# Optimization experiments

Hardware: AMD Instinct MI355X
Metric: run time of the kernel (lower is better)

The kernel has to match this reference:

```python
import jax, jax.numpy as jnp
import numpy as np

B, L, DIM = 16, 4096, 512
N_FFT, HOP, WIN = 1024, 256, 1024
PAD = (WIN - HOP) // 2  # 'same' padding trim
OUT_DIM = N_FFT + 2


def hann_window(win):
    n = jnp.arange(win, dtype=jnp.float32)
    return 0.5 - 0.5 * jnp.cos(2.0 * jnp.pi * n / win)


def setup_inputs() -> dict:
    key = jax.random.key(0)
    k1, k2 = jax.random.split(key)
    x = jax.random.normal(k1, (B, L, DIM), dtype=jnp.float32)
    W = jax.random.normal(k2, (OUT_DIM, DIM), dtype=jnp.float32) * 0.02
    b = jnp.zeros((OUT_DIM,), dtype=jnp.float32)
    return {"x": x, "W": W, "b": b}


def _istft(S):
    # S: (B, N_FFT//2+1, T) complex rfft spectrum
    T = S.shape[-1]
    frames = jnp.fft.irfft(S, n=N_FFT, axis=1)
    window = hann_window(WIN)
    frames = frames * window[None, :, None]
    out_len = (T - 1) * HOP + WIN
    idx = jnp.arange(T)[:, None] * HOP + jnp.arange(WIN)[None, :]
    fr = frames.transpose(0, 2, 1)
    y = jnp.zeros((fr.shape[0], out_len), fr.dtype).at[:, idx].add(fr)
    env = jnp.zeros((out_len,), fr.dtype).at[idx].add(
        jnp.broadcast_to(window * window, idx.shape))
    y = y[:, PAD:out_len - PAD]
    env = env[PAD:out_len - PAD]
    return y / env


def reference(x, W, b):
    # Linear projection: (B, L, DIM) -> (B, L, N_FFT+2)
    h = jnp.einsum('bld,od->blo', x, W) + b
    h = h.transpose(0, 2, 1)                              # (B, N_FFT+2, L)
    mag, p = jnp.split(h, 2, axis=1)                      # each (B, N_FFT//2+1, L)
    mag = jnp.minimum(jnp.exp(mag), 100.0)                # exp + clip(max=100)
    S = mag * jax.lax.complex(jnp.cos(p), jnp.sin(p))
    return _istft(S)                                      # (B, L*HOP)
```

## Files before the change

### kernel.cpp

```cpp
#include <hip/hip_runtime.h>
#include <hip/hip_bf16.h>
#include <math.h>

#define BATCH   16
#define TFRM    4096
#define DIM     512
#define NFFT    1024
#define HOP     256
#define PADC    384
#define MROWS   (BATCH*TFRM)
#define OUTLEN  1048576
#define TWO_PI_OVER_N 0.006135923151542565f
#define INV_TWO_PI    0.15915494309189535f

typedef __bf16 bf16x8 __attribute__((ext_vector_type(8)));
typedef float  f32x4  __attribute__((ext_vector_type(4)));

__device__ __forceinline__ ushort f2bf(float f) {
  union { float f; unsigned u; } v; v.f = f;
  unsigned u = v.u;
  unsigned r = (u + 0x7FFFu + ((u >> 16) & 1u)) >> 16;
  return (ushort)r;
}
__device__ __forceinline__ float bf2f(ushort h) {
  union { unsigned u; float f; } v; v.u = ((unsigned)h) << 16;
  return v.f;
}
__device__ __forceinline__ float fast_sin(float x) { return __builtin_amdgcn_sinf(x * INV_TWO_PI); }
__device__ __forceinline__ float fast_cos(float x) { return __builtin_amdgcn_cosf(x * INV_TWO_PI); }
__device__ __forceinline__ float fast_exp(float x) { return __builtin_amdgcn_exp2f(x * 1.4426950408889634f); }
__device__ __forceinline__ float dpp_xor1(float v) {
  return __int_as_float(__builtin_amdgcn_update_dpp(
      __float_as_int(v), __float_as_int(v), 0xB1, 0xF, 0xF, false));
}

__global__ void k_prep_x(const float* __restrict__ x, const float* __restrict__ W,
                         const float* __restrict__ bias,
                         ushort* __restrict__ xbf, float* __restrict__ s512) {
  const int row  = blockIdx.x * 4 + (threadIdx.x >> 6);
  const int lane = threadIdx.x & 63;
  const float* xr = x + (size_t)row * DIM + lane * 8;
  float4 v0 = *(const float4*)xr;
  float4 v1 = *(const float4*)(xr + 4);
  ushort4 u0, u1;
  u0.x = f2bf(v0.x); u0.y = f2bf(v0.y); u0.z = f2bf(v0.z); u0.w = f2bf(v0.w);
  u1.x = f2bf(v1.x); u1.y = f2bf(v1.y); u1.z = f2bf(v1.z); u1.w = f2bf(v1.w);
  ushort* xo = xbf + (size_t)row * DIM + lane * 8;
  *(ushort4*)xo = u0;
  *(ushort4*)(xo + 4) = u1;
  const float* w0 = W + 512 * DIM + lane * 8;
  const float* w1 = W + 1025 * DIM + lane * 8;
  float4 a0 = *(const float4*)w0, a1 = *(const float4*)(w0 + 4);
  float4 b0 = *(const float4*)w1, b1 = *(const float4*)(w1 + 4);
  float sm = v0.x*a0.x + v0.y*a0.y + v0.z*a0.z + v0.w*a0.w
           + v1.x*a1.x + v1.y*a1.y + v1.z*a1.z + v1.w*a1.w;
  float sp = v0.x*b0.x + v0.y*b0.y + v0.z*b0.z + v0.w*b0.w
           + v1.x*b1.x + v1.y*b1.y + v1.z*b1.z + v1.w*b1.w;
#pragma unroll
  for (int off = 32; off; off >>= 1) {
    sm += __shfl_down(sm, off);
    sp += __shfl_down(sp, off);
  }
  if (lane == 0) {
    float mag = fminf(fast_exp(sm + bias[512]), 100.0f);
    s512[row] = mag * fast_cos(sp + bias[1025]) * (1.0f / 1024.0f);
  }
}

__global__ void k_prep_w(const float* __restrict__ W, ushort* __restrict__ o) {
  int i = blockIdx.x * 256 + threadIdx.x;
  int r = i >> 9;
  int c = i & 511;
  int orig = (r >> 1) + (r & 1) * 513;
  o[i] = f2bf(W[orig * DIM + c]);
}

__global__ void k_basis(ushort* __restrict__ basE, ushort* __restrict__ basO) {
  int r = blockIdx.x;
  int n = r + 1;
  for (int k = threadIdx.x; k < 512; k += 256) {
    float e, o;
    if (k == 0) { e = 1.0f / 1024.0f; o = 0.0f; }
    else {
      int ph = (k * n) & 1023;
      float ang = (float)ph * TWO_PI_OVER_N;
      e = 2.0f * cosf(ang) * (1.0f / 1024.0f);
      o = 2.0f * sinf(ang) * (1.0f / 1024.0f);
    }
    basE[r * 512 + k] = f2bf(e);
    basO[r * 512 + k] = f2bf(o);
  }
}

template<int EPI>
__global__ __launch_bounds__(256) void k_gemm(const ushort* A, const ushort* A2, int lda,
                                              const ushort* Bt, const ushort* Bt2, int ldb,
                                              ushort* C, ushort* C2, int ldc,
                                              int nbn, int NK, int nsplit,
                                              const float* __restrict__ bias,
                                              const float* __restrict__ s512) {
  __shared__ __align__(16) ushort lds[3][2][128 * 32];
  const int tid  = threadIdx.x;
  const int cpx  = gridDim.x >> 3;
  int bid  = (blockIdx.x & 7) * cpx + (blockIdx.x >> 3);
  bool second = false;
  if (nsplit > 0 && bid >= nsplit) { second = true; A = A2; Bt = Bt2; C = C2; bid -= nsplit; }
  const int bm   = bid / nbn;
  const int bn   = bid - bm * nbn;
  const int lane = tid & 63;
  const int wv   = tid >> 6;
  const int wr   = (wv >> 1) * 64;
  const int wc   = (wv & 1) * 64;
  const int lr   = lane & 15;
  const int gx   = ((lane >> 4) ^ ((lane >> 1) & 3)) << 3;

  f32x4 acc[4][4] = {};

  const int swz = ((tid & 3) ^ ((tid >> 3) & 3)) << 3;
  auto stage = [&](const ushort* __restrict__ g, int ld, int row0, int k0, ushort* l) {
#pragma unroll
    for (int p = 0; p < 2; ++p) {
      int i = tid + p * 256;
      const ushort* gp = g + (size_t)(row0 + (i >> 2)) * ld + k0 + swz;
      ushort* lp = l + ((i >> 6) << 9);
      __builtin_amdgcn_global_load_lds(
          (const __attribute__((address_space(1))) void*)gp,
          (__attribute__((address_space(3))) void*)lp, 16, 0, 0);
    }
  };

  stage(A,  lda, bm * 128, 0,  &lds[0][0][0]);
  stage(Bt, ldb, bn * 128, 0,  &lds[0][1][0]);
  stage(A,  lda, bm * 128, 32, &lds[1][0][0]);
  stage(Bt, ldb, bn * 128, 32, &lds[1][1][0]);
  asm volatile("s_waitcnt vmcnt(4)" ::: "memory");
  __syncthreads();

  int sl = 0;
  for (int t = 0; t < NK; ++t) {
    if (t + 2 < NK) {
      const int psl = (sl >= 1) ? sl - 1 : 2;
      stage(A,  lda, bm * 128, (t + 2) << 5, &lds[psl][0][0]);
      stage(Bt, ldb, bn * 128, (t + 2) << 5, &lds[psl][1][0]);
    }
    const ushort* lA = &lds[sl][0][0];
    const ushort* lB = &lds[sl][1][0];
    bf16x8 aF[4], bF[4];
#pragma unroll
    for (int m = 0; m < 4; ++m)
      aF[m] = *(const bf16x8*)(lA + (wr + m * 16 + lr) * 32 + gx);
#pragma unroll
    for (int n = 0; n < 4; ++n)
      bF[n] = *(const bf16x8*)(lB + (wc + n * 16 + lr) * 32 + gx);
#pragma unroll
    for (int m = 0; m < 4; ++m)
#pragma unroll
      for (int n = 0; n < 4; ++n)
        acc[m][n] = __builtin_amdgcn_mfma_f32_16x16x32_bf16(aF[m], bF[n], acc[m][n], 0, 0, 0);
    if (t + 2 < NK)      asm volatile("s_waitcnt vmcnt(4)" ::: "memory");
    else if (t + 2 == NK) asm volatile("s_waitcnt vmcnt(0)" ::: "memory");
    if (t + 1 < NK) __syncthreads();
    sl = (sl >= 2) ? 0 : sl + 1;
  }

  const int rl = wr + ((lane >> 4) << 2);
  const int r0 = bm * 128 + rl;
  ushort* epi = &lds[0][0][0];
  __syncthreads();

  if constexpr (EPI == 0) {
#pragma unroll
    for (int m = 0; m < 4; ++m) {
      float4 sv4 = {0.f, 0.f, 0.f, 0.f};
      if (!second) sv4 = *(const float4*)(s512 + r0 + m * 16);
#pragma unroll
      for (int j = 0; j < 4; ++j) {
        float sv = ((const float*)&sv4)[j];
        int row = rl + m * 16 + j;
#pragma unroll
        for (int n = 0; n < 4; ++n) {
          int c = wc + n * 16 + lr;
          float par = second ? 0.0f : ((c & 1) ? sv : -sv);
          epi[row * 144 + c] = f2bf(acc[m][n][j] + par);
        }
      }
    }
    __syncthreads();
#pragma unroll
    for (int i = 0; i < 8; ++i) {
      int row = (tid >> 4) + i * 16;
      int co  = (tid & 15) << 3;
      bf16x8 v = *(const bf16x8*)(epi + row * 144 + co);
      *(bf16x8*)(C + (size_t)(bm * 128 + row) * ldc + bn * 128 + co) = v;
    }
  } else {
    ushort* tA = epi;
    ushort* tB = epi + 128 * 80;
#pragma unroll
    for (int m = 0; m < 4; ++m) {
#pragma unroll
      for (int n = 0; n < 4; ++n) {
        const int cl  = wc + n * 16 + lr;
        const int kk  = (bn * 128 + cl) >> 1;
        const bool isPhase = (cl & 1);
        const float bs = bias[isPhase ? 513 + kk : kk];
        ushort* dst = (isPhase ? tB : tA);
        const int kkl = cl >> 1;
#pragma unroll
        for (int j = 0; j < 4; ++j) {
          float v = acc[m][n][j] + bs;
          float pv = dpp_xor1(v);
          float hm = isPhase ? pv : v;
          float hp = isPhase ? v : pv;
          float mag = fminf(fast_exp(hm), 100.0f);
          float outv = isPhase ? mag * fast_sin(hp) : mag * fast_cos(hp);
          dst[(rl + m * 16 + j) * 80 + kkl] = f2bf(outv);
        }
      }
    }
    __syncthreads();
#pragma unroll
    for (int i = 0; i < 4; ++i) {
      int row = (tid >> 3) + i * 32;
      int co  = (tid & 7) << 3;
      size_t go = (size_t)(bm * 128 + row) * ldc + bn * 64 + co;
      bf16x8 va = *(const bf16x8*)(tA + row * 80 + co);
      *(bf16x8*)(C + go) = va;
      bf16x8 vb = *(const bf16x8*)(tB + row * 80 + co);
      *(bf16x8*)(C2 + go) = vb;
    }
  }
}

__global__ void k_oa(const ushort* __restrict__ E, const ushort* __restrict__ O,
                     float* __restrict__ out) {
  int u = blockIdx.x * 256 + threadIdx.x;
  int b  = u >> 18;
  int g  = u & 262143;
  int s  = (g << 2) + PADC;
  int t0 = s >> 8;
  int nb = s & 255;
  float acc[4] = {0.f, 0.f, 0.f, 0.f};
  bool interior = (t0 >= 3) && (t0 < TFRM);
  float env[4];
#pragma unroll
  for (int j = 0; j < 4; ++j) env[j] = interior ? 1.5f : 0.0f;
#pragma unroll
  for (int q = 0; q < 4; ++q) {
    int t = t0 - q;
    if (t < 0 || t >= TFRM) continue;
    int n = nb + (q << 8);
    size_t base = ((size_t)(b << 12) + t) << 9;
    float w[4];
#pragma unroll
    for (int j = 0; j < 4; ++j) {
      w[j] = 0.5f - 0.5f * __builtin_amdgcn_cosf((float)(n + j) * (1.0f / 1024.0f));
      if (!interior) env[j] += w[j] * w[j];
    }
    float d[4];
    if (n <= 508) {
      ushort4 e1 = *(const ushort4*)(E + base + n);
      ushort4 o1 = *(const ushort4*)(O + base + n);
      if (n >= 4) {
        ushort4 e0 = *(const ushort4*)(E + base + n - 4);
        ushort4 o0 = *(const ushort4*)(O + base + n - 4);
        d[0] = bf2f(e0.w) - bf2f(o0.w);
      } else d[0] = 0.0f;
      d[1] = bf2f(e1.x) - bf2f(o1.x);
      d[2] = bf2f(e1.y) - bf2f(o1.y);
      d[3] = bf2f(e1.z) - bf2f(o1.z);
    } else if (n == 512) {
      ushort4 e = *(const ushort4*)(E + base + 508);
      ushort4 o = *(const ushort4*)(O + base + 508);
      d[0] = bf2f(e.w) - bf2f(o.w);
      d[1] = bf2f(e.z) + bf2f(o.z);
      d[2] = bf2f(e.y) + bf2f(o.y);
      d[3] = bf2f(e.x) + bf2f(o.x);
    } else {
      ushort4 e = *(const ushort4*)(E + base + 1020 - n);
      ushort4 o = *(const ushort4*)(O + base + 1020 - n);
      d[0] = bf2f(e.w) + bf2f(o.w);
      d[1] = bf2f(e.z) + bf2f(o.z);
      d[2] = bf2f(e.y) + bf2f(o.y);
      d[3] = bf2f(e.x) + bf2f(o.x);
    }
#pragma unroll
    for (int j = 0; j < 4; ++j) acc[j] += w[j] * d[j];
  }
  float4 o4;
  o4.x = acc[0] / env[0]; o4.y = acc[1] / env[1];
  o4.z = acc[2] / env[2]; o4.w = acc[3] / env[3];
  *(float4*)(out + (size_t)u * 4) = o4;
}

extern "C" void kernel_launch(void* const* d_in, const int* in_sizes, int n_in,
                              void* d_out, int out_size, void* d_ws, size_t ws_size,
                              hipStream_t stream) {
  const float* x    = (const float*)d_in[0];
  const float* W    = (const float*)d_in[1];
  const float* bias = (const float*)d_in[2];
  float* out = (float*)d_out;
  char* ws = (char*)d_ws;

  ushort* xbf  = (ushort*)(ws + 0);
  ushort* Epp  = (ushort*)(ws + 0);
  ushort* h_a  = (ushort*)(ws + 67108864);
  ushort* h_b  = (ushort*)(ws + 134217728);
  ushort* Obuf = (ushort*)(ws + 201326592);
  ushort* Wp   = (ushort*)(ws + 268435456);
  ushort* basE = (ushort*)(ws + 269484032);
  ushort* basO = (ushort*)(ws + 270008320);
  float*  s512 = (float*) (ws + 270532608);

  k_prep_x<<<MROWS / 4, 256, 0, stream>>>(x, W, bias, xbf, s512);
  k_prep_w<<<(1024 * 512) / 256, 256, 0, stream>>>(W, Wp);
  k_basis<<<512, 256, 0, stream>>>(basE, basO);

  k_gemm<1><<<(MROWS / 128) * 8, 256, 0, stream>>>(
      xbf, nullptr, DIM, Wp, nullptr, DIM, h_a, h_b, 512, 8, 16, 0, bias, nullptr);

  k_gemm<0><<<2 * (MROWS / 128) * 4, 256, 0, stream>>>(
      h_a, h_b, 512, basE, basO, 512, Epp, Obuf, 512, 4, 16, (MROWS / 128) * 4,
      nullptr, s512);

  k_oa<<<(BATCH * OUTLEN) / 1024, 256, 0, stream>>>(Epp, Obuf, out);
}
```

Before: 294.1 us.

## Load GEMM B operand straight to registers, stage only A through LDS

The B tile is no longer staged through shared memory. Each wave loads its B fragments directly from global memory into registers, double-buffered across two k-steps, while A keeps its three-slot LDS pipeline. The main loop is unrolled by two so the even and odd B register buffers alternate. This halves LDS traffic and the shared-memory footprint, which may raise occupancy, at the cost of more global/L2 reads for B (the two wave rows load the same B columns), more registers, and an assumption that NK is even.

```diff
diff --git a/kernel.cpp b/kernel.cpp
--- a/kernel.cpp
+++ b/kernel.cpp
@@ -99,7 +99,7 @@
                                               int nbn, int NK, int nsplit,
                                               const float* __restrict__ bias,
                                               const float* __restrict__ s512) {
-  __shared__ __align__(16) ushort lds[3][2][128 * 32];
+  __shared__ __align__(16) ushort lds[20480];
   const int tid  = threadIdx.x;
   const int cpx  = gridDim.x >> 3;
   int bid  = (blockIdx.x & 7) * cpx + (blockIdx.x >> 3);
@@ -117,55 +117,73 @@
   f32x4 acc[4][4] = {};
 
   const int swz = ((tid & 3) ^ ((tid >> 3) & 3)) << 3;
-  auto stage = [&](const ushort* __restrict__ g, int ld, int row0, int k0, ushort* l) {
-#pragma unroll
-    for (int p = 0; p < 2; ++p) {
-      int i = tid + p * 256;
-      const ushort* gp = g + (size_t)(row0 + (i >> 2)) * ld + k0 + swz;
-      ushort* lp = l + ((i >> 6) << 9);
-      __builtin_amdgcn_global_load_lds(
-          (const __attribute__((address_space(1))) void*)gp,
-          (__attribute__((address_space(3))) void*)lp, 16, 0, 0);
-    }
+  const ushort* gA = A + (size_t)(bm * 128 + (tid >> 2)) * lda + swz;
+  auto stageA = [&](int t, int slot) {
+    const ushort* g0 = gA + t * 32;
+    ushort* l = &lds[slot * 4096] + ((tid >> 6) << 9);
+    __builtin_amdgcn_global_load_lds(
+        (const __attribute__((address_space(1))) void*)g0,
+        (__attribute__((address_space(3))) void*)l, 16, 0, 0);
+    __builtin_amdgcn_global_load_lds(
+        (const __attribute__((address_space(1))) void*)(g0 + (size_t)64 * lda),
+        (__attribute__((address_space(3))) void*)(l + 2048), 16, 0, 0);
   };
 
-  stage(A,  lda, bm * 128, 0,  &lds[0][0][0]);
-  stage(Bt, ldb, bn * 128, 0,  &lds[0][1][0]);
-  stage(A,  lda, bm * 128, 32, &lds[1][0][0]);
-  stage(Bt, ldb, bn * 128, 32, &lds[1][1][0]);
-  asm volatile("s_waitcnt vmcnt(4)" ::: "memory");
+  const ushort* gB = Bt + (size_t)(bn * 128 + wc + lr) * ldb + ((lane >> 4) << 3);
+  auto loadB = [&](int t, bf16x8* bf) {
+#pragma unroll
+    for (int n = 0; n < 4; ++n)
+      bf[n] = *(const bf16x8*)(gB + (size_t)(n * 16) * ldb + t * 32);
+  };
+
+  bf16x8 bE[4], bO[4];
+
+  stageA(0, 0); loadB(0, bE);
+  asm volatile("" ::: "memory");
+  stageA(1, 1); loadB(1, bO);
+  asm volatile("s_waitcnt vmcnt(6)" ::: "memory");
   __syncthreads();
 
   int sl = 0;
-  for (int t = 0; t < NK; ++t) {
-    if (t + 2 < NK) {
-      const int psl = (sl >= 1) ? sl - 1 : 2;
-      stage(A,  lda, bm * 128, (t + 2) << 5, &lds[psl][0][0]);
-      stage(Bt, ldb, bn * 128, (t + 2) << 5, &lds[psl][1][0]);
-    }
-    const ushort* lA = &lds[sl][0][0];
-    const ushort* lB = &lds[sl][1][0];
-    bf16x8 aF[4], bF[4];
-#pragma unroll
-    for (int m = 0; m < 4; ++m)
-      aF[m] = *(const bf16x8*)(lA + (wr + m * 16 + lr) * 32 + gx);
-#pragma unroll
-    for (int n = 0; n < 4; ++n)
-      bF[n] = *(const bf16x8*)(lB + (wc + n * 16 + lr) * 32 + gx);
-#pragma unroll
-    for (int m = 0; m < 4; ++m)
-#pragma unroll
-      for (int n = 0; n < 4; ++n)
-        acc[m][n] = __builtin_amdgcn_mfma_f32_16x16x32_bf16(aF[m], bF[n], acc[m][n], 0, 0, 0);
-    if (t + 2 < NK)      asm volatile("s_waitcnt vmcnt(4)" ::: "memory");
-    else if (t + 2 == NK) asm volatile("s_waitcnt vmcnt(0)" ::: "memory");
-    if (t + 1 < NK) __syncthreads();
-    sl = (sl >= 2) ? 0 : sl + 1;
+  for (int t = 0; t < NK; t += 2) {
+    const int s0 = sl;
+    const int s1 = (s0 >= 2) ? s0 - 2 : s0 + 1;
+#pragma unroll
+    for (int h = 0; h < 2; ++h) {
+      const int u = t + h;
+      const int su = h ? s1 : s0;
+      const int sp = h ? s0 : ((s0 >= 1) ? s0 - 1 : 2);
+      const ushort* lA = &lds[su * 4096];
+      bf16x8 aF[4];
+#pragma unroll
+      for (int m = 0; m < 4; ++m)
+        aF[m] = *(const bf16x8*)(lA + (wr + m * 16 + lr) * 32 + gx);
+      if (u + 2 < NK) stageA(u + 2, sp);
+      if (h == 0) {
+#pragma unroll
+        for (int m = 0; m < 4; ++m)
+#pragma unroll
+          for (int n = 0; n < 4; ++n)
+            acc[m][n] = __builtin_amdgcn_mfma_f32_16x16x32_bf16(aF[m], bE[n], acc[m][n], 0, 0, 0);
+        if (u + 2 < NK) loadB(u + 2, bE);
+      } else {
+#pragma unroll
+        for (int m = 0; m < 4; ++m)
+#pragma unroll
+          for (int n = 0; n < 4; ++n)
+            acc[m][n] = __builtin_amdgcn_mfma_f32_16x16x32_bf16(aF[m], bO[n], acc[m][n], 0, 0, 0);
+        if (u + 2 < NK) loadB(u + 2, bO);
+      }
+      if (u + 2 < NK)      asm volatile("s_waitcnt vmcnt(6)" ::: "memory");
+      else if (u + 1 < NK) asm volatile("s_waitcnt vmcnt(0)" ::: "memory");
+      if (u + 1 < NK) __syncthreads();
+    }
+    sl = (s1 >= 2) ? s1 - 2 : s1 + 1;
   }
 
   const int rl = wr + ((lane >> 4) << 2);
   const int r0 = bm * 128 + rl;
-  ushort* epi = &lds[0][0][0];
+  ushort* epi = lds;
   __syncthreads();
 
   if constexpr (EPI == 0) {
```

New measurement: 405.4 us. 1.38x slower.
